# Kernel tuning notes

Measured on AMD Instinct MI355X. Metric: run time of the kernel, lower is better.

## Reference

```python
import jax, jax.numpy as jnp
import numpy as np

D_MODEL = 1024
N_HEADS = 16
HEAD_DIM = D_MODEL // N_HEADS
ROPE_BASE = 10000.0
B, S = 2, 2048


def _rope_cos_sin(seq_len):
    inv_freq = 1.0 / (ROPE_BASE ** (jnp.arange(0, HEAD_DIM, 2, dtype=jnp.float32) / HEAD_DIM))
    t = jnp.arange(seq_len, dtype=jnp.float32)
    freqs = jnp.outer(t, inv_freq)                 # [S, HEAD_DIM/2]
    emb = jnp.concatenate([freqs, freqs], axis=-1)  # [S, HEAD_DIM]
    return jnp.cos(emb), jnp.sin(emb)


def _apply_rope(x, cos, sin):
    # x: [B, H, S, D]; cos/sin: [S, D]
    x1 = x[..., ::2]
    x2 = x[..., 1::2]
    return jnp.concatenate(
        [x1 * cos[..., ::2] - x2 * sin[..., ::2],
         x1 * sin[..., 1::2] + x2 * cos[..., 1::2]], axis=-1)


def setup_inputs() -> dict:
    key = jax.random.key(0)
    ks = jax.random.split(key, 5)
    std = 1.0 / np.sqrt(D_MODEL)
    x = jax.random.normal(ks[0], (B, S, D_MODEL), dtype=jnp.float32)
    Wq = jax.random.normal(ks[1], (D_MODEL, D_MODEL), dtype=jnp.float32) * std
    Wk = jax.random.normal(ks[2], (D_MODEL, D_MODEL), dtype=jnp.float32) * std
    Wv = jax.random.normal(ks[3], (D_MODEL, D_MODEL), dtype=jnp.float32) * std
    Wo = jax.random.normal(ks[4], (D_MODEL, D_MODEL), dtype=jnp.float32) * std
    attn_mask = jnp.tril(jnp.ones((S, S), dtype=jnp.int32))  # 0 = masked (causal)
    return {"x": x, "Wq": Wq, "Wk": Wk, "Wv": Wv, "Wo": Wo, "attn_mask": attn_mask}


def reference(x, Wq, Wk, Wv, Wo, attn_mask):
    b, s, _ = x.shape
    scale = 1.0 / np.sqrt(HEAD_DIM)
    # torch Linear: y = x @ W.T
    q = (x @ Wq.T).reshape(b, s, N_HEADS, HEAD_DIM).transpose(0, 2, 1, 3)
    k = (x @ Wk.T).reshape(b, s, N_HEADS, HEAD_DIM).transpose(0, 2, 1, 3)
    v = (x @ Wv.T).reshape(b, s, N_HEADS, HEAD_DIM).transpose(0, 2, 1, 3)
    cos, sin = _rope_cos_sin(s)
    q = _apply_rope(q, cos, sin)
    k = _apply_rope(k, cos, sin)
    scores = jnp.einsum('bhqd,bhkd->bhqk', q, k) * scale  # [B,H,S,S]
    scores = jnp.where(attn_mask == 0, -jnp.inf, scores)
    attn = jax.nn.softmax(scores, axis=-1)
    out = jnp.einsum('bhqk,bhkd->bhqd', attn, v)
    out = out.transpose(0, 2, 1, 3).reshape(b, s, D_MODEL)
    return out @ Wo.T
```

## Files before the change

### kernel.cpp

```cpp
#include <hip/hip_runtime.h>
#include <hip/hip_bf16.h>
#include <cstdint>

#define SEQ 2048
#define NH  16
#define HD  64
#define DM  1024
#define BATCH 2

typedef unsigned short ushort_t;
typedef __attribute__((ext_vector_type(8))) short short8;
typedef __attribute__((ext_vector_type(4))) float f32x4;

__device__ __forceinline__ ushort_t f2bf(float f){
  __hip_bfloat16 h = __float2bfloat16(f);
  return *reinterpret_cast<ushort_t*>(&h);
}
__device__ __forceinline__ ushort_t f2bf_fast(float f){
  uint32_t u = __float_as_uint(f);
  u += 0x7FFF + ((u >> 16) & 1);
  return (ushort_t)(u >> 16);
}

#define GLDS(g, l) __builtin_amdgcn_global_load_lds( \
    (const __attribute__((address_space(1))) void*)(g), \
    (__attribute__((address_space(3))) void*)(l), 16, 0, 0)

__global__ __launch_bounds__(256) void rope_tab_kernel(float* __restrict__ tab){
  int idx = blockIdx.x * 256 + threadIdx.x;
  int t = idx >> 5, j = idx & 31;
  float invf = exp2f(-(float)j * 0.41524101186092033f);
  float sn, cn;
  sincosf((float)t * invf, &sn, &cn);
  tab[2*idx]   = cn;
  tab[2*idx+1] = sn;
}

__global__ __launch_bounds__(256) void cvt_kernel(
    const float* __restrict__ x,  const float* __restrict__ Wq,
    const float* __restrict__ Wk, const float* __restrict__ Wv,
    const float* __restrict__ Wo,
    ushort_t* __restrict__ xb,  ushort_t* __restrict__ wqb,
    ushort_t* __restrict__ wkb, ushort_t* __restrict__ wvb,
    ushort_t* __restrict__ wob)
{
  int f = blockIdx.x * 256 + threadIdx.x;
  const float* s; ushort_t* d; int off;
  if(f < (1<<20)){ s = x; d = xb; off = f; }
  else{
    int r = f - (1<<20);
    int w = r >> 18;
    off = r & ((1<<18)-1);
    s = (w==0)?Wq:(w==1)?Wk:(w==2)?Wv:Wo;
    d = (w==0)?wqb:(w==1)?wkb:(w==2)?wvb:wob;
  }
  float4 v = *reinterpret_cast<const float4*>(s + (size_t)off*4);
  ushort_t t[4] = {f2bf(v.x), f2bf(v.y), f2bf(v.z), f2bf(v.w)};
  *reinterpret_cast<uint2*>(d + (size_t)off*4) = *reinterpret_cast<const uint2*>(t);
}

template<bool SWAP>
__device__ __forceinline__ void gemm_core_bf16_glds(
    const ushort_t* __restrict__ A, const ushort_t* __restrict__ B,
    ushort_t* As, ushort_t* Bs,
    int m0, int n0, f32x4 acc[4][4])
{
  const int tid  = threadIdx.x;
  const int lane = tid & 63;
  const int wave = tid >> 6;
  const int quad = lane >> 4, l16 = lane & 15;
  const int wm = (wave >> 1) * 64, wn = (wave & 1) * 64;

  const int srow0 = tid >> 2, sseg0 = tid & 3;

  #define STAGE_BF16(k0, hb) { \
    _Pragma("unroll") \
    for(int u = 0; u < 2; u++){ \
      int idx = tid + u * 256; \
      int row = srow0 + u * 64, seg = sseg0; \
      int col = (seg ^ (row & 3)) * 8; \
      ushort_t* la = &As[(hb)*4096 + (size_t)(idx & ~63) * 8]; \
      ushort_t* lb = &Bs[(hb)*4096 + (size_t)(idx & ~63) * 8]; \
      GLDS(&A[(size_t)(m0+row)*DM + (k0) + col], la); \
      GLDS(&B[(size_t)(n0+row)*DM + (k0) + col], lb); \
    } }

  STAGE_BF16(0, 0);
  __syncthreads();
  int cur = 0;
  for(int k0 = 0; k0 < DM; k0 += 32){
    if(k0 + 32 < DM) STAGE_BF16(k0 + 32, cur ^ 1);
    const ushort_t* as = &As[cur*4096];
    const ushort_t* bs = &Bs[cur*4096];
    short8 af[4], bf[4];
    #pragma unroll
    for(int mt=0;mt<4;mt++){
      int row = wm + mt*16 + l16;
      af[mt] = *reinterpret_cast<const short8*>(&as[row*32 + (quad ^ (row&3))*8]);
    }
    #pragma unroll
    for(int nt=0;nt<4;nt++){
      int row = wn + nt*16 + l16;
      bf[nt] = *reinterpret_cast<const short8*>(&bs[row*32 + (quad ^ (row&3))*8]);
    }
    #pragma unroll
    for(int mt=0;mt<4;mt++)
      #pragma unroll
      for(int nt=0;nt<4;nt++)
        acc[mt][nt] = SWAP
          ? __builtin_amdgcn_mfma_f32_16x16x32_bf16(bf[nt], af[mt], acc[mt][nt], 0, 0, 0)
          : __builtin_amdgcn_mfma_f32_16x16x32_bf16(af[mt], bf[nt], acc[mt][nt], 0, 0, 0);
    __syncthreads();
    cur ^= 1;
  }
  #undef STAGE_BF16
}

template<bool SWAP>
__device__ __forceinline__ void gemm_core_f32(
    const float* __restrict__ A, const float* __restrict__ B,
    ushort_t* As, ushort_t* Bs, int m0, int n0, f32x4 acc[4][4])
{
  const int tid  = threadIdx.x;
  const int lane = tid & 63;
  const int wave = tid >> 6;
  const int quad = lane >> 4, l16 = lane & 15;
  const int wm = (wave >> 1) * 64, wn = (wave & 1) * 64;
  for(int k0 = 0; k0 < DM; k0 += 32){
    #pragma unroll
    for(int u = 0; u < 4; u++){
      int idx = tid + u * 256;
      int row = idx >> 3, seg = idx & 7;
      float4 av = *reinterpret_cast<const float4*>(&A[(size_t)(m0+row)*DM + k0 + seg*4]);
      float4 bv = *reinterpret_cast<const float4*>(&B[(size_t)(n0+row)*DM + k0 + seg*4]);
      ushort_t at[4] = {f2bf(av.x), f2bf(av.y), f2bf(av.z), f2bf(av.w)};
      ushort_t bt[4] = {f2bf(bv.x), f2bf(bv.y), f2bf(bv.z), f2bf(bv.w)};
      *reinterpret_cast<uint2*>(&As[row*40 + seg*4]) = *reinterpret_cast<const uint2*>(at);
      *reinterpret_cast<uint2*>(&Bs[row*40 + seg*4]) = *reinterpret_cast<const uint2*>(bt);
    }
    __syncthreads();
    short8 af[4], bf[4];
    #pragma unroll
    for(int mt=0;mt<4;mt++) af[mt] = *reinterpret_cast<const short8*>(&As[(wm+mt*16+l16)*40 + quad*8]);
    #pragma unroll
    for(int nt=0;nt<4;nt++) bf[nt] = *reinterpret_cast<const short8*>(&Bs[(wn+nt*16+l16)*40 + quad*8]);
    #pragma unroll
    for(int mt=0;mt<4;mt++)
      #pragma unroll
      for(int nt=0;nt<4;nt++)
        acc[mt][nt] = SWAP
          ? __builtin_amdgcn_mfma_f32_16x16x32_bf16(bf[nt], af[mt], acc[mt][nt], 0, 0, 0)
          : __builtin_amdgcn_mfma_f32_16x16x32_bf16(af[mt], bf[nt], acc[mt][nt], 0, 0, 0);
    __syncthreads();
  }
}

__device__ __forceinline__ void qkv_epilogue(
    int z, int m0, int n0, f32x4 acc[4][4], const float* __restrict__ tab,
    ushort_t* __restrict__ Q, ushort_t* __restrict__ Ko, ushort_t* __restrict__ Vt)
{
  const int tid  = threadIdx.x;
  const int lane = tid & 63;
  const int wave = tid >> 6;
  const int quad = lane >> 4, l16 = lane & 15;
  const int wm = (wave >> 1) * 64, wn = (wave & 1) * 64;
  if(z < 2){
    ushort_t* outp = (z == 0) ? Q : Ko;
    const float qscale = (z == 0) ? 0.125f : 1.0f;
    #pragma unroll
    for(int nt=0;nt<4;nt++){
      int n  = n0 + wn + nt*16 + l16;
      int h  = n >> 6, dh = n & 63;
      int j  = dh & 31;
      int outd = (dh >> 1) + (dh & 1) * 32;
      bool even = (dh & 1) == 0;
      #pragma unroll
      for(int mt=0;mt<4;mt++){
        #pragma unroll
        for(int r=0;r<4;r++){
          int m = m0 + wm + mt*16 + quad*4 + r;
          int b = m >> 11, s = m & 2047;
          float v = acc[mt][nt][r];
          float p = __shfl_xor(v, 1);
          float2 cs = *reinterpret_cast<const float2*>(&tab[(s*32 + j)*2]);
          float o = even ? (v * cs.x - p * cs.y) : (p * cs.y + v * cs.x);
          outp[((size_t)(b*NH + h)*SEQ + s)*HD + outd] = f2bf(o * qscale);
        }
      }
    }
  } else {
    #pragma unroll
    for(int nt=0;nt<4;nt++){
      #pragma unroll
      for(int mt=0;mt<4;mt++){
        int m = m0 + wm + mt*16 + l16;
        int b = m >> 11, s = m & 2047;
        #pragma unroll
        for(int r=0;r<4;r++){
          int n = n0 + wn + nt*16 + quad*4 + r;
          int h = n >> 6, dh = n & 63;
          Vt[((size_t)(b*NH + h)*HD + dh)*SEQ + s] = f2bf_fast(acc[mt][nt][r]);
        }
      }
    }
  }
}

__global__ __launch_bounds__(256) void qkv_bf16_kernel(
    const ushort_t* __restrict__ xb,
    const ushort_t* __restrict__ wqb, const ushort_t* __restrict__ wkb,
    const ushort_t* __restrict__ wvb, const float* __restrict__ tab,
    ushort_t* __restrict__ Q, ushort_t* __restrict__ Ko, ushort_t* __restrict__ Vt)
{
  const int z = blockIdx.z;
  const ushort_t* W = (z == 0) ? wqb : (z == 1) ? wkb : wvb;
  const int m0 = blockIdx.x * 128, n0 = blockIdx.y * 128;
  __shared__ __align__(16) ushort_t As[2*128*32];
  __shared__ __align__(16) ushort_t Bs[2*128*32];
  f32x4 acc[4][4];
  #pragma unroll
  for(int i=0;i<4;i++)
    #pragma unroll
    for(int j=0;j<4;j++) acc[i][j] = (f32x4){0.f,0.f,0.f,0.f};
  if(z == 2) gemm_core_bf16_glds<true >(xb, W, As, Bs, m0, n0, acc);
  else       gemm_core_bf16_glds<false>(xb, W, As, Bs, m0, n0, acc);
  qkv_epilogue(z, m0, n0, acc, tab, Q, Ko, Vt);
}

__global__ __launch_bounds__(256) void qkv_f32_kernel(
    const float* __restrict__ x,
    const float* __restrict__ Wq, const float* __restrict__ Wk,
    const float* __restrict__ Wv, const float* __restrict__ tab,
    ushort_t* __restrict__ Q, ushort_t* __restrict__ Ko, ushort_t* __restrict__ Vt)
{
  const int z = blockIdx.z;
  const float* W = (z == 0) ? Wq : (z == 1) ? Wk : Wv;
  const int m0 = blockIdx.x * 128, n0 = blockIdx.y * 128;
  __shared__ __align__(16) char smem[20480];
  ushort_t* As = (ushort_t*)smem;
  ushort_t* Bs = (ushort_t*)(smem + 10240);
  f32x4 acc[4][4];
  #pragma unroll
  for(int i=0;i<4;i++)
    #pragma unroll
    for(int j=0;j<4;j++) acc[i][j] = (f32x4){0.f,0.f,0.f,0.f};
  if(z == 2) gemm_core_f32<true >(x, W, As, Bs, m0, n0, acc);
  else       gemm_core_f32<false>(x, W, As, Bs, m0, n0, acc);
  qkv_epilogue(z, m0, n0, acc, tab, Q, Ko, Vt);
}

__global__ __launch_bounds__(256) void attn_kernel(
    ushort_t* __restrict__ Qbuf, const ushort_t* __restrict__ K,
    const ushort_t* __restrict__ Vt)
{
  const int bh = blockIdx.x;
  const int y  = blockIdx.y;
  const int g  = (y < 8) ? (15 - y) : (y - 8);
  const int T  = 2*(g+1);
  const int tid  = threadIdx.x;
  const int lane = tid & 63;
  const int wave = tid >> 6;
  const int quad = lane >> 4, l16 = lane & 15;

  ushort_t*       Qp = Qbuf + (size_t)bh * SEQ * HD;
  const ushort_t* Kp = K    + (size_t)bh * SEQ * HD;
  const ushort_t* Vp = Vt   + (size_t)bh * HD * SEQ;

  __shared__ __align__(16) ushort_t Ks[64*72];
  __shared__ __align__(16) ushort_t Vs[64*72];
  __shared__ __align__(16) ushort_t Pl[4][32*72];
  ushort_t* pl = &Pl[wave][0];

  const int srow0 = tid >> 3;
  const int scol  = (tid & 7) * 8;

  const int q0w = 128*g + 32*wave;

  short8 qf[2][2];
  #pragma unroll
  for(int s=0;s<2;s++)
    #pragma unroll
    for(int kk=0;kk<2;kk++)
      qf[s][kk] = *reinterpret_cast<const short8*>(&Qp[(size_t)(q0w + 16*s + l16)*HD + kk*32 + quad*8]);

  f32x4 oacc[2][4];
  #pragma unroll
  for(int s=0;s<2;s++)
    #pragma unroll
    for(int dt=0;dt<4;dt++) oacc[s][dt] = (f32x4){0.f,0.f,0.f,0.f};
  float llane[2] = {0.f, 0.f};

  uint4 kreg[2], vreg[2];
  #pragma unroll
  for(int u=0;u<2;u++){
    int row = srow0 + u*32;
    kreg[u] = *reinterpret_cast<const uint4*>(&Kp[(size_t)row*HD + scol]);
    vreg[u] = *reinterpret_cast<const uint4*>(&Vp[(size_t)row*SEQ + scol]);
  }

  for(int t = 0; t < T; t++){
    const int kv0 = t * 64;

    __syncthreads();
    #pragma unroll
    for(int u=0;u<2;u++){
      int row = srow0 + u*32;
      *reinterpret_cast<uint4*>(&Ks[row*72 + scol]) = kreg[u];
      *reinterpret_cast<uint4*>(&Vs[row*72 + scol]) = vreg[u];
    }
    __syncthreads();

    if(t < T-1){
      #pragma unroll
      for(int u=0;u<2;u++){
        int row = srow0 + u*32;
        kreg[u] = *reinterpret_cast<const uint4*>(&Kp[(size_t)(kv0 + 64 + row)*HD + scol]);
        vreg[u] = *reinterpret_cast<const uint4*>(&Vp[(size_t)row*SEQ + kv0 + 64 + scol]);
      }
    }

    short8 kf[4][2], vf[4][2];
    #pragma unroll
    for(int nt=0;nt<4;nt++)
      #pragma unroll
      for(int kk=0;kk<2;kk++)
        kf[nt][kk] = *reinterpret_cast<const short8*>(&Ks[(nt*16 + l16)*72 + kk*32 + quad*8]);
    #pragma unroll
    for(int dt=0;dt<4;dt++)
      #pragma unroll
      for(int kk=0;kk<2;kk++)
        vf[dt][kk] = *reinterpret_cast<const short8*>(&Vs[(dt*16 + l16)*72 + kk*32 + quad*8]);

    #pragma unroll
    for(int s=0;s<2;s++){
      f32x4 sacc[4];
      #pragma unroll
      for(int nt=0;nt<4;nt++) sacc[nt] = (f32x4){0.f,0.f,0.f,0.f};
      #pragma unroll
      for(int kk=0;kk<2;kk++)
        #pragma unroll
        for(int nt=0;nt<4;nt++)
          sacc[nt] = __builtin_amdgcn_mfma_f32_16x16x32_bf16(kf[nt][kk], qf[s][kk], sacc[nt], 0,0,0);

      const int q_abs = q0w + 16*s + l16;
      const bool maskable = (kv0 + 63 > q0w + 16*s);
      float pv[4][4];
      #pragma unroll
      for(int nt=0;nt<4;nt++)
        #pragma unroll
        for(int r=0;r<4;r++){
          float sv = sacc[nt][r];
          if(maskable){
            int kv_abs = kv0 + nt*16 + quad*4 + r;
            sv = (kv_abs > q_abs) ? -1e30f : sv;
          }
          float p = __expf(sv);
          pv[nt][r] = p;
          llane[s] += p;
        }

      asm volatile("" ::: "memory");
      #pragma unroll
      for(int nt=0;nt<4;nt++){
        uint32_t lo = (uint32_t)f2bf_fast(pv[nt][0]) | ((uint32_t)f2bf_fast(pv[nt][1]) << 16);
        uint32_t hi = (uint32_t)f2bf_fast(pv[nt][2]) | ((uint32_t)f2bf_fast(pv[nt][3]) << 16);
        uint2 pk; pk.x = lo; pk.y = hi;
        *reinterpret_cast<uint2*>(&pl[(16*s + l16)*72 + nt*16 + quad*4]) = pk;
      }
      asm volatile("s_waitcnt lgkmcnt(0)" ::: "memory");

      #pragma unroll
      for(int kk=0;kk<2;kk++){
        short8 pf = *reinterpret_cast<const short8*>(&pl[(16*s + l16)*72 + kk*32 + quad*8]);
        #pragma unroll
        for(int dt=0;dt<4;dt++)
          oacc[s][dt] = __builtin_amdgcn_mfma_f32_16x16x32_bf16(vf[dt][kk], pf, oacc[s][dt], 0,0,0);
      }
    }
  }

  #pragma unroll
  for(int s=0;s<2;s++){
    float lt = llane[s];
    lt += __shfl_xor(lt, 16);
    lt += __shfl_xor(lt, 32);
    float inv = 1.0f / lt;
    #pragma unroll
    for(int dt=0;dt<4;dt++){
      uint32_t lo = (uint32_t)f2bf_fast(oacc[s][dt][0] * inv) | ((uint32_t)f2bf_fast(oacc[s][dt][1] * inv) << 16);
      uint32_t hi = (uint32_t)f2bf_fast(oacc[s][dt][2] * inv) | ((uint32_t)f2bf_fast(oacc[s][dt][3] * inv) << 16);
      uint2 pk; pk.x = lo; pk.y = hi;
      *reinterpret_cast<uint2*>(&Qp[(size_t)(q0w + 16*s + l16)*HD + dt*16 + quad*4]) = pk;
    }
  }
}

__global__ __launch_bounds__(256) void out_proj_bf16_kernel(
    const ushort_t* __restrict__ ctx, const ushort_t* __restrict__ wob,
    float* __restrict__ out)
{
  const int m0 = blockIdx.x * 128, n0 = blockIdx.y * 128;
  __shared__ __align__(16) ushort_t As[2*128*32];
  __shared__ __align__(16) ushort_t Bs[2*128*32];
  const int tid  = threadIdx.x;
  const int lane = tid & 63;
  const int wave = tid >> 6;
  const int quad = lane >> 4, l16 = lane & 15;
  const int wm = (wave >> 1) * 64, wn = (wave & 1) * 64;
  const int srow0 = tid >> 2, sseg0 = tid & 3;

  f32x4 acc[4][4];
  #pragma unroll
  for(int i=0;i<4;i++)
    #pragma unroll
    for(int j=0;j<4;j++) acc[i][j] = (f32x4){0.f,0.f,0.f,0.f};

  #define STAGE_OP(k0, hb) { \
    const int head = (k0) >> 6, off = (k0) & 63; \
    _Pragma("unroll") \
    for(int u = 0; u < 2; u++){ \
      int idx = tid + u * 256; \
      int row = srow0 + u * 64, seg = sseg0; \
      int col = (seg ^ (row & 3)) * 8; \
      int m = m0 + row, b = m >> 11, s = m & 2047; \
      ushort_t* la = &As[(hb)*4096 + (size_t)(idx & ~63) * 8]; \
      ushort_t* lb = &Bs[(hb)*4096 + (size_t)(idx & ~63) * 8]; \
      GLDS(&ctx[((size_t)(b*NH + head)*SEQ + s)*HD + off + col], la); \
      GLDS(&wob[(size_t)(n0+row)*DM + (k0) + col], lb); \
    } }

  STAGE_OP(0, 0);
  __syncthreads();
  int cur = 0;
  for(int k0 = 0; k0 < DM; k0 += 32){
    if(k0 + 32 < DM) STAGE_OP(k0 + 32, cur ^ 1);
    const ushort_t* as = &As[cur*4096];
    const ushort_t* bs = &Bs[cur*4096];
    short8 af[4], bf[4];
    #pragma unroll
    for(int mt=0;mt<4;mt++){
      int row = wm + mt*16 + l16;
      af[mt] = *reinterpret_cast<const short8*>(&as[row*32 + (quad ^ (row&3))*8]);
    }
    #pragma unroll
    for(int nt=0;nt<4;nt++){
      int row = wn + nt*16 + l16;
      bf[nt] = *reinterpret_cast<const short8*>(&bs[row*32 + (quad ^ (row&3))*8]);
    }
    #pragma unroll
    for(int mt=0;mt<4;mt++)
      #pragma unroll
      for(int nt=0;nt<4;nt++)
        acc[mt][nt] = __builtin_amdgcn_mfma_f32_16x16x32_bf16(af[mt], bf[nt], acc[mt][nt], 0, 0, 0);
    __syncthreads();
    cur ^= 1;
  }
  #undef STAGE_OP

  #pragma unroll
  for(int mt=0;mt<4;mt++)
    #pragma unroll
    for(int nt=0;nt<4;nt++)
      #pragma unroll
      for(int r=0;r<4;r++){
        int m = m0 + wm + mt*16 + quad*4 + r;
        int n = n0 + wn + nt*16 + l16;
        out[(size_t)m*DM + n] = acc[mt][nt][r];
      }
}

__global__ __launch_bounds__(256) void out_proj_f32_kernel(
    const ushort_t* __restrict__ ctx, const float* __restrict__ Wo,
    float* __restrict__ out)
{
  const int m0 = blockIdx.x * 128, n0 = blockIdx.y * 128;
  __shared__ __align__(16) ushort_t As[128*40];
  __shared__ __align__(16) ushort_t Bs[128*40];
  const int tid  = threadIdx.x;
  const int lane = tid & 63;
  const int wave = tid >> 6;
  const int quad = lane >> 4, l16 = lane & 15;
  const int wm = (wave >> 1) * 64, wn = (wave & 1) * 64;

  f32x4 acc[4][4];
  #pragma unroll
  for(int i=0;i<4;i++)
    #pragma unroll
    for(int j=0;j<4;j++) acc[i][j] = (f32x4){0.f,0.f,0.f,0.f};

  for(int k0 = 0; k0 < DM; k0 += 32){
    const int head = k0 >> 6, off = k0 & 63;
    #pragma unroll
    for(int u = 0; u < 2; u++){
      int idx = tid + u * 256;
      int row = idx >> 2, seg = idx & 3;
      int m = m0 + row, b = m >> 11, s = m & 2047;
      *reinterpret_cast<uint4*>(&As[row*40 + seg*8]) =
        *reinterpret_cast<const uint4*>(&ctx[((size_t)(b*NH + head)*SEQ + s)*HD + off + seg*8]);
    }
    #pragma unroll
    for(int u = 0; u < 4; u++){
      int idx = tid + u * 256;
      int row = idx >> 3, seg = idx & 7;
      float4 bv = *reinterpret_cast<const float4*>(&Wo[(size_t)(n0+row)*DM + k0 + seg*4]);
      ushort_t bt[4] = {f2bf(bv.x), f2bf(bv.y), f2bf(bv.z), f2bf(bv.w)};
      *reinterpret_cast<uint2*>(&Bs[row*40 + seg*4]) = *reinterpret_cast<const uint2*>(bt);
    }
    __syncthreads();
    short8 af[4], bf[4];
    #pragma unroll
    for(int mt=0;mt<4;mt++) af[mt] = *reinterpret_cast<const short8*>(&As[(wm+mt*16+l16)*40 + quad*8]);
    #pragma unroll
    for(int nt=0;nt<4;nt++) bf[nt] = *reinterpret_cast<const short8*>(&Bs[(wn+nt*16+l16)*40 + quad*8]);
    #pragma unroll
    for(int mt=0;mt<4;mt++)
      #pragma unroll
      for(int nt=0;nt<4;nt++)
        acc[mt][nt] = __builtin_amdgcn_mfma_f32_16x16x32_bf16(af[mt], bf[nt], acc[mt][nt], 0, 0, 0);
    __syncthreads();
  }
  #pragma unroll
  for(int mt=0;mt<4;mt++)
    #pragma unroll
    for(int nt=0;nt<4;nt++)
      #pragma unroll
      for(int r=0;r<4;r++){
        int m = m0 + wm + mt*16 + quad*4 + r;
        int n = n0 + wn + nt*16 + l16;
        out[(size_t)m*DM + n] = acc[mt][nt][r];
      }
}

extern "C" void kernel_launch(void* const* d_in, const int* in_sizes, int n_in,
                              void* d_out, int out_size, void* d_ws, size_t ws_size,
                              hipStream_t stream) {
  const float* x  = (const float*)d_in[0];
  const float* Wq = (const float*)d_in[1];
  const float* Wk = (const float*)d_in[2];
  const float* Wv = (const float*)d_in[3];
  const float* Wo = (const float*)d_in[4];
  float* out = (float*)d_out;

  char* ws = (char*)d_ws;
  ushort_t* Qb  = (ushort_t*)ws;
  float*    tab = (float*)(ws + (8u << 20));
  ushort_t* Kb  = (ushort_t*)d_out;
  ushort_t* Vt  = (ushort_t*)d_out + (size_t)BATCH*NH*SEQ*HD;

  rope_tab_kernel<<<256, 256, 0, stream>>>(tab);

  const bool big_ws = ws_size >= (25u << 20);

  if(big_ws){
    ushort_t* xb  = (ushort_t*)(ws + (8u  << 20) + (512u << 10));
    char*     wb0 = ws + (16u << 20) + (512u << 10);
    ushort_t* wqb = (ushort_t*)(wb0);
    ushort_t* wkb = (ushort_t*)(wb0 + (2u << 20));
    ushort_t* wvb = (ushort_t*)(wb0 + (4u << 20));
    ushort_t* wob = (ushort_t*)(wb0 + (6u << 20));
    cvt_kernel<<<8192, 256, 0, stream>>>(x, Wq, Wk, Wv, Wo, xb, wqb, wkb, wvb, wob);
    dim3 g1(32, 8, 3);
    qkv_bf16_kernel<<<g1, 256, 0, stream>>>(xb, wqb, wkb, wvb, tab, Qb, Kb, Vt);
    dim3 g2(32, 16);
    attn_kernel<<<g2, 256, 0, stream>>>(Qb, Kb, Vt);
    dim3 g3(32, 8);
    out_proj_bf16_kernel<<<g3, 256, 0, stream>>>(Qb, wob, out);
  } else {
    dim3 g1(32, 8, 3);
    qkv_f32_kernel<<<g1, 256, 0, stream>>>(x, Wq, Wk, Wv, tab, Qb, Kb, Vt);
    dim3 g2(32, 16);
    attn_kernel<<<g2, 256, 0, stream>>>(Qb, Kb, Vt);
    dim3 g3(32, 8);
    out_proj_f32_kernel<<<g3, 256, 0, stream>>>(Qb, Wo, out);
  }
}
```

Measured before the change: 240.6 us.

## Fuse RoPE table into prep kernel and vectorize swapped QKV epilogue

Folds the RoPE cos/sin table generation into the conversion kernel as extra blocks, which removes one kernel launch on the main path. The table is transposed to a [j][s] layout. Q/K projections now use the swapped MFMA operand order, so each lane holds four consecutive head dims for one row. The epilogue can then apply RoPE without cross-lane shuffles and write packed 32-bit bf16 pairs using fast rounding, in place of scattered 16-bit stores.

```diff
diff --git a/kernel.cpp b/kernel.cpp
--- a/kernel.cpp
+++ b/kernel.cpp
@@ -26,9 +26,8 @@
     (const __attribute__((address_space(1))) void*)(g), \
     (__attribute__((address_space(3))) void*)(l), 16, 0, 0)
 
-__global__ __launch_bounds__(256) void rope_tab_kernel(float* __restrict__ tab){
-  int idx = blockIdx.x * 256 + threadIdx.x;
-  int t = idx >> 5, j = idx & 31;
+__device__ __forceinline__ void rope_tab_elem(float* __restrict__ tab, int idx){
+  int t = idx & 2047, j = idx >> 11;
   float invf = exp2f(-(float)j * 0.41524101186092033f);
   float sn, cn;
   sincosf((float)t * invf, &sn, &cn);
@@ -36,15 +35,24 @@
   tab[2*idx+1] = sn;
 }
 
-__global__ __launch_bounds__(256) void cvt_kernel(
+__global__ __launch_bounds__(256) void rope_tab_kernel(float* __restrict__ tab){
+  rope_tab_elem(tab, blockIdx.x * 256 + threadIdx.x);
+}
+
+__global__ __launch_bounds__(256) void prep_kernel(
     const float* __restrict__ x,  const float* __restrict__ Wq,
     const float* __restrict__ Wk, const float* __restrict__ Wv,
     const float* __restrict__ Wo,
     ushort_t* __restrict__ xb,  ushort_t* __restrict__ wqb,
     ushort_t* __restrict__ wkb, ushort_t* __restrict__ wvb,
-    ushort_t* __restrict__ wob)
-{
-  int f = blockIdx.x * 256 + threadIdx.x;
+    ushort_t* __restrict__ wob, float* __restrict__ tab)
+{
+  int bid = blockIdx.x;
+  if(bid >= 8192){
+    rope_tab_elem(tab, (bid - 8192) * 256 + threadIdx.x);
+    return;
+  }
+  int f = bid * 256 + threadIdx.x;
   const float* s; ushort_t* d; int off;
   if(f < (1<<20)){ s = x; d = xb; off = f; }
   else{
@@ -155,37 +163,42 @@
   }
 }
 
-__device__ __forceinline__ void qkv_epilogue(
+__device__ __forceinline__ void qkv_epilogue_swap(
     int z, int m0, int n0, f32x4 acc[4][4], const float* __restrict__ tab,
     ushort_t* __restrict__ Q, ushort_t* __restrict__ Ko, ushort_t* __restrict__ Vt)
 {
-  const int tid  = threadIdx.x;
-  const int lane = tid & 63;
-  const int wave = tid >> 6;
+  const int lane = threadIdx.x & 63;
+  const int wave = threadIdx.x >> 6;
   const int quad = lane >> 4, l16 = lane & 15;
   const int wm = (wave >> 1) * 64, wn = (wave & 1) * 64;
   if(z < 2){
     ushort_t* outp = (z == 0) ? Q : Ko;
     const float qscale = (z == 0) ? 0.125f : 1.0f;
     #pragma unroll
-    for(int nt=0;nt<4;nt++){
-      int n  = n0 + wn + nt*16 + l16;
-      int h  = n >> 6, dh = n & 63;
-      int j  = dh & 31;
-      int outd = (dh >> 1) + (dh & 1) * 32;
-      bool even = (dh & 1) == 0;
-      #pragma unroll
-      for(int mt=0;mt<4;mt++){
-        #pragma unroll
-        for(int r=0;r<4;r++){
-          int m = m0 + wm + mt*16 + quad*4 + r;
-          int b = m >> 11, s = m & 2047;
-          float v = acc[mt][nt][r];
-          float p = __shfl_xor(v, 1);
-          float2 cs = *reinterpret_cast<const float2*>(&tab[(s*32 + j)*2]);
-          float o = even ? (v * cs.x - p * cs.y) : (p * cs.y + v * cs.x);
-          outp[((size_t)(b*NH + h)*SEQ + s)*HD + outd] = f2bf(o * qscale);
-        }
+    for(int mt=0;mt<4;mt++){
+      int m = m0 + wm + mt*16 + l16;
+      int b = m >> 11, s = m & 2047;
+      #pragma unroll
+      for(int nt=0;nt<4;nt++){
+        int nbase = n0 + wn + nt*16 + quad*4;
+        int h  = nbase >> 6, dhb = nbase & 63;
+        int jb = dhb & 31;
+        float v0 = acc[mt][nt][0], v1 = acc[mt][nt][1];
+        float v2 = acc[mt][nt][2], v3 = acc[mt][nt][3];
+        float2 cs0 = *reinterpret_cast<const float2*>(&tab[((jb  )*SEQ + s)*2]);
+        float2 cs1 = *reinterpret_cast<const float2*>(&tab[((jb+1)*SEQ + s)*2]);
+        float2 cs2 = *reinterpret_cast<const float2*>(&tab[((jb+2)*SEQ + s)*2]);
+        float2 cs3 = *reinterpret_cast<const float2*>(&tab[((jb+3)*SEQ + s)*2]);
+        float oe0 = (v0*cs0.x - v1*cs0.y) * qscale;
+        float oo0 = (v0*cs1.y + v1*cs1.x) * qscale;
+        float oe1 = (v2*cs2.x - v3*cs2.y) * qscale;
+        float oo1 = (v2*cs3.y + v3*cs3.x) * qscale;
+        int d2 = dhb >> 1;
+        size_t base = ((size_t)(b*NH + h)*SEQ + s)*HD;
+        uint32_t lo = (uint32_t)f2bf_fast(oe0) | ((uint32_t)f2bf_fast(oe1) << 16);
+        uint32_t hi = (uint32_t)f2bf_fast(oo0) | ((uint32_t)f2bf_fast(oo1) << 16);
+        *reinterpret_cast<uint32_t*>(&outp[base + d2])      = lo;
+        *reinterpret_cast<uint32_t*>(&outp[base + d2 + 32]) = hi;
       }
     }
   } else {
@@ -222,9 +235,8 @@
   for(int i=0;i<4;i++)
     #pragma unroll
     for(int j=0;j<4;j++) acc[i][j] = (f32x4){0.f,0.f,0.f,0.f};
-  if(z == 2) gemm_core_bf16_glds<true >(xb, W, As, Bs, m0, n0, acc);
-  else       gemm_core_bf16_glds<false>(xb, W, As, Bs, m0, n0, acc);
-  qkv_epilogue(z, m0, n0, acc, tab, Q, Ko, Vt);
+  gemm_core_bf16_glds<true>(xb, W, As, Bs, m0, n0, acc);
+  qkv_epilogue_swap(z, m0, n0, acc, tab, Q, Ko, Vt);
 }
 
 __global__ __launch_bounds__(256) void qkv_f32_kernel(
@@ -244,9 +256,8 @@
   for(int i=0;i<4;i++)
     #pragma unroll
     for(int j=0;j<4;j++) acc[i][j] = (f32x4){0.f,0.f,0.f,0.f};
-  if(z == 2) gemm_core_f32<true >(x, W, As, Bs, m0, n0, acc);
-  else       gemm_core_f32<false>(x, W, As, Bs, m0, n0, acc);
-  qkv_epilogue(z, m0, n0, acc, tab, Q, Ko, Vt);
+  gemm_core_f32<true>(x, W, As, Bs, m0, n0, acc);
+  qkv_epilogue_swap(z, m0, n0, acc, tab, Q, Ko, Vt);
 }
 
 __global__ __launch_bounds__(256) void attn_kernel(
@@ -547,8 +558,6 @@
   ushort_t* Kb  = (ushort_t*)d_out;
   ushort_t* Vt  = (ushort_t*)d_out + (size_t)BATCH*NH*SEQ*HD;
 
-  rope_tab_kernel<<<256, 256, 0, stream>>>(tab);
-
   const bool big_ws = ws_size >= (25u << 20);
 
   if(big_ws){
@@ -558,7 +567,7 @@
     ushort_t* wkb = (ushort_t*)(wb0 + (2u << 20));
     ushort_t* wvb = (ushort_t*)(wb0 + (4u << 20));
     ushort_t* wob = (ushort_t*)(wb0 + (6u << 20));
-    cvt_kernel<<<8192, 256, 0, stream>>>(x, Wq, Wk, Wv, Wo, xb, wqb, wkb, wvb, wob);
+    prep_kernel<<<8448, 256, 0, stream>>>(x, Wq, Wk, Wv, Wo, xb, wqb, wkb, wvb, wob, tab);
     dim3 g1(32, 8, 3);
     qkv_bf16_kernel<<<g1, 256, 0, stream>>>(xb, wqb, wkb, wvb, tab, Qb, Kb, Vt);
     dim3 g2(32, 16);
@@ -566,6 +575,7 @@
     dim3 g3(32, 8);
     out_proj_bf16_kernel<<<g3, 256, 0, stream>>>(Qb, wob, out);
   } else {
+    rope_tab_kernel<<<256, 256, 0, stream>>>(tab);
     dim3 g1(32, 8, 3);
     qkv_f32_kernel<<<g1, 256, 0, stream>>>(x, Wq, Wk, Wv, tab, Qb, Kb, Vt);
     dim3 g2(32, 16);
```

Result: no change. 238.4 us (-0.9%).
